# Kernel optimization log

Hardware: AMD Instinct MI355X
Metric: run time of the kernel (lower is better)

Reference implementation:

```python
import jax, jax.numpy as jnp
import numpy as np

S, B, H, E, V, L = 64, 32, 1024, 512, 32000, 2


def setup_inputs() -> dict:
    key = jax.random.key(0)
    ks = jax.random.split(key, 12)
    dl = 1.0 / float(np.sqrt(H))
    u = lambda k, shape, a: jax.random.uniform(k, shape, minval=-a, maxval=a, dtype=jnp.float32)
    return {
        "inputs": jax.random.randint(ks[0], (S, B), 0, V),            # token ids [seq, batch]
        "hidden": jnp.zeros((L, B, H), jnp.float32),                  # init_hidden()
        "emb_W": u(ks[1], (V, E), 0.1),                               # embedding, uniform(-0.1,0.1)
        "Wx0": u(ks[2], (H, E), dl), "Wh0": u(ks[3], (H, H), dl), "bh0": u(ks[4], (H,), dl),
        "Wx1": u(ks[5], (H, H), dl), "Wh1": u(ks[6], (H, H), dl), "bh1": u(ks[7], (H,), dl),
        "Wout": u(ks[8], (V, H), 0.1),                                # output Linear, uniform(-0.1,0.1)
        "bout": jnp.zeros((V,), jnp.float32),                         # output bias zeros
    }


def reference(inputs, hidden, emb_W, Wx0, Wh0, bh0, Wx1, Wh1, bh1, Wout, bout):
    # Embedding lookup for all timesteps (dropout is identity at dp_keep_prob=1.0)
    x = emb_W[inputs]  # [S, B, E]
    Wxs = (Wx0, Wx1)
    Whs = (Wh0, Wh1)
    bs = (bh0, bh1)

    def step(h, x_t):
        # h: [L, B, H]; x_t: [B, E]
        out = x_t
        new_h = []
        for j in range(L):  # fixed small number of structurally distinct layers
            hj = jnp.tanh(out @ Wxs[j].T + h[j] @ Whs[j].T + bs[j])  # vanilla tanh RNN cell
            new_h.append(hj)
            out = hj
        return jnp.stack(new_h), out

    hidden_final, tops = jax.lax.scan(step, hidden, x)  # tops: [S, B, H]
    logits = tops @ Wout.T + bout                        # [S, B, V]
    return logits, hidden_final
```

## Files before the change

### kernel.cpp

```cpp
#include <hip/hip_runtime.h>
#include <hip/hip_bf16.h>

#define S_ 64
#define B_ 32
#define H_ 1024
#define E_ 512
#define V_ 32000

typedef unsigned short ushort_t;
typedef __attribute__((ext_vector_type(8))) short short8;
typedef __attribute__((ext_vector_type(4))) float f32x4;

__device__ __forceinline__ ushort_t f32_bf16(float x) {
    union { float f; unsigned u; } v; v.f = x;
    unsigned r = v.u + 0x7FFF + ((v.u >> 16) & 1);
    return (ushort_t)(r >> 16);
}

__device__ __forceinline__ float bf16_f32(ushort_t x) {
    union { unsigned u; float f; } v; v.u = ((unsigned)x) << 16;
    return v.f;
}

__global__ void cvt_bf16(const float* __restrict__ src, ushort_t* __restrict__ dst, int n4) {
    int i = blockIdx.x * blockDim.x + threadIdx.x;
    int stride = gridDim.x * blockDim.x;
    const float4* s4 = (const float4*)src;
    ushort4* d4 = (ushort4*)dst;
    for (; i < n4; i += stride) {
        float4 v = s4[i];
        ushort4 o;
        o.x = f32_bf16(v.x); o.y = f32_bf16(v.y);
        o.z = f32_bf16(v.z); o.w = f32_bf16(v.w);
        d4[i] = o;
    }
}

__global__ void init_hidden(const float* __restrict__ hid,
                            ushort_t* __restrict__ h0buf, ushort_t* __restrict__ h1buf) {
    int i = blockIdx.x * blockDim.x + threadIdx.x;
    int j = i & (B_ * H_ - 1);
    if (i < B_ * H_) h0buf[B_ * H_ + j] = f32_bf16(hid[i]);
    else             h1buf[B_ * H_ + j] = f32_bf16(hid[i]);
}

__global__ void gather_emb(const int* __restrict__ tok, const float* __restrict__ emb,
                           ushort_t* __restrict__ xb) {
    int m = blockIdx.x;
    int t = tok[m];
    const float4* src = (const float4*)(emb + (long)t * E_);
    ushort4* dst = (ushort4*)(xb + (long)m * E_);
    int i = threadIdx.x;
    float4 v = src[i];
    ushort4 o;
    o.x = f32_bf16(v.x); o.y = f32_bf16(v.y);
    o.z = f32_bf16(v.z); o.w = f32_bf16(v.w);
    dst[i] = o;
}

__global__ __launch_bounds__(256) void xproj_kernel(const ushort_t* __restrict__ Xb,
                                                    const ushort_t* __restrict__ Wx0b,
                                                    const float* __restrict__ bh0,
                                                    float* __restrict__ xproj) {
    int wid = (blockIdx.x * 256 + threadIdx.x) >> 6;
    int lane = threadIdx.x & 63;
    int quad = lane >> 4;
    int nt = wid & 63, mt = wid >> 6;
    int mrow = mt * 16 + (lane & 15);
    int nrow = nt * 16 + (lane & 15);
    const short8* Ap = (const short8*)(Xb + (long)mrow * E_ + quad * 8);
    const short8* Bp = (const short8*)(Wx0b + (long)nrow * E_ + quad * 8);
    f32x4 acc = {0.f, 0.f, 0.f, 0.f};
#pragma unroll
    for (int k = 0; k < E_ / 32; ++k)
        acc = __builtin_amdgcn_mfma_f32_16x16x32_bf16(Ap[k * 4], Bp[k * 4], acc, 0, 0, 0);
    float bias = bh0[nrow];
#pragma unroll
    for (int r = 0; r < 4; ++r) {
        int m = mt * 16 + quad * 4 + r;
        xproj[(long)m * H_ + nrow] = acc[r] + bias;
    }
}

__global__ __launch_bounds__(256) void step_kernel(const ushort_t* __restrict__ Wh0b,
                                                   const ushort_t* __restrict__ Wx1b,
                                                   const ushort_t* __restrict__ Wh1b,
                                                   const float* __restrict__ bh1,
                                                   const float* __restrict__ xproj,
                                                   ushort_t* __restrict__ h0buf,
                                                   ushort_t* __restrict__ h1buf,
                                                   ushort_t* __restrict__ tops,
                                                   int p) {
    int lb = blockIdx.x;
    int lane = threadIdx.x & 63;
    int widx = threadIdx.x >> 6;
    int quad = lane >> 4;
    if (lb < 32) {
        if (p >= S_) return;
        int wid = lb * 4 + widx;
        int nt = wid & 63, mt = wid >> 6;
        int b0 = mt * 16 + (lane & 15);
        int h = nt * 16 + (lane & 15);
        const ushort_t* Aprev = h0buf + ((p + 1) & 1) * (B_ * H_);
        const short8* Ap = (const short8*)(Aprev + (long)b0 * H_ + quad * 8);
        const short8* Wp = (const short8*)(Wh0b + (long)h * H_ + quad * 8);
        f32x4 acc = {0.f, 0.f, 0.f, 0.f};
#pragma unroll
        for (int k = 0; k < H_ / 32; ++k)
            acc = __builtin_amdgcn_mfma_f32_16x16x32_bf16(Ap[k * 4], Wp[k * 4], acc, 0, 0, 0);
        ushort_t* out = h0buf + (p & 1) * (B_ * H_);
        const float* xp = xproj + (long)p * B_ * H_;
#pragma unroll
        for (int r = 0; r < 4; ++r) {
            int b = mt * 16 + quad * 4 + r;
            float v = tanhf(acc[r] + xp[b * H_ + h]);
            out[b * H_ + h] = f32_bf16(v);
        }
    } else {
        if (p < 1) return;
        int t = p - 1;
        int wid = (lb - 32) * 4 + widx;
        int nt = wid & 63, mt = wid >> 6;
        int b0 = mt * 16 + (lane & 15);
        int h = nt * 16 + (lane & 15);
        const ushort_t* A0 = h0buf + (t & 1) * (B_ * H_);
        const ushort_t* A1 = h1buf + ((t + 1) & 1) * (B_ * H_);
        const short8* Ap0 = (const short8*)(A0 + (long)b0 * H_ + quad * 8);
        const short8* Wp0 = (const short8*)(Wx1b + (long)h * H_ + quad * 8);
        const short8* Ap1 = (const short8*)(A1 + (long)b0 * H_ + quad * 8);
        const short8* Wp1 = (const short8*)(Wh1b + (long)h * H_ + quad * 8);
        f32x4 acc = {0.f, 0.f, 0.f, 0.f};
#pragma unroll
        for (int k = 0; k < H_ / 32; ++k)
            acc = __builtin_amdgcn_mfma_f32_16x16x32_bf16(Ap0[k * 4], Wp0[k * 4], acc, 0, 0, 0);
#pragma unroll
        for (int k = 0; k < H_ / 32; ++k)
            acc = __builtin_amdgcn_mfma_f32_16x16x32_bf16(Ap1[k * 4], Wp1[k * 4], acc, 0, 0, 0);
        float bias = bh1[h];
        ushort_t* out = h1buf + (t & 1) * (B_ * H_);
        ushort_t* top = tops + (long)t * B_ * H_;
#pragma unroll
        for (int r = 0; r < 4; ++r) {
            int b = mt * 16 + quad * 4 + r;
            float v = tanhf(acc[r] + bias);
            ushort_t bv = f32_bf16(v);
            out[b * H_ + h] = bv;
            top[b * H_ + h] = bv;
        }
    }
}

#define BM 128
#define BN 128
#define BK 32

__device__ __forceinline__ void ld_lds16(const ushort_t* g, ushort_t* l) {
    __builtin_amdgcn_global_load_lds((const __attribute__((address_space(1))) void*)g,
                                     (__attribute__((address_space(3))) void*)l, 16, 0, 0);
}

__global__ __launch_bounds__(256) void out_gemm(const ushort_t* __restrict__ A,
                                                const ushort_t* __restrict__ Bw,
                                                const float* __restrict__ bout,
                                                float* __restrict__ C) {
    __shared__ __align__(16) ushort_t lA[BM * BK];
    __shared__ __align__(16) ushort_t lB[BN * BK];
    int mblk = blockIdx.x;
    int nblk = blockIdx.y;
    int tid = threadIdx.x;
    int lane = tid & 63;
    int w = tid >> 6;
    int quad = lane >> 4;
    int srow = tid >> 2;
    int skol = (tid & 3) * 8;
    const ushort_t* Ag = A + (long)(mblk * BM + srow) * H_ + skol;
    const ushort_t* Bg = Bw + (long)(nblk * BN + srow) * H_ + skol;
    ushort_t* lA0 = lA + tid * 8;
    ushort_t* lA1 = lA + 2048 + tid * 8;
    ushort_t* lB0 = lB + tid * 8;
    ushort_t* lB1 = lB + 2048 + tid * 8;

    int msub = (w & 1) * 64;
    int nsub = (w >> 1) * 64;
    f32x4 acc[4][4];
#pragma unroll
    for (int i = 0; i < 4; ++i)
#pragma unroll
        for (int j = 0; j < 4; ++j) acc[i][j] = (f32x4){0.f, 0.f, 0.f, 0.f};

    for (int k0 = 0; k0 < H_; k0 += BK) {
        ld_lds16(Ag + k0, lA0);
        ld_lds16(Ag + 64 * H_ + k0, lA1);
        ld_lds16(Bg + k0, lB0);
        ld_lds16(Bg + 64 * H_ + k0, lB1);
        __syncthreads();
        short8 af[4], bf[4];
#pragma unroll
        for (int i = 0; i < 4; ++i)
            af[i] = *(const short8*)&lA[(msub + i * 16 + (lane & 15)) * BK + quad * 8];
#pragma unroll
        for (int j = 0; j < 4; ++j)
            bf[j] = *(const short8*)&lB[(nsub + j * 16 + (lane & 15)) * BK + quad * 8];
#pragma unroll
        for (int i = 0; i < 4; ++i)
#pragma unroll
            for (int j = 0; j < 4; ++j)
                acc[i][j] = __builtin_amdgcn_mfma_f32_16x16x32_bf16(af[i], bf[j], acc[i][j], 0, 0, 0);
        __syncthreads();
    }

#pragma unroll
    for (int j = 0; j < 4; ++j) {
        int n = nblk * BN + nsub + j * 16 + (lane & 15);
        float bo = bout[n];
#pragma unroll
        for (int i = 0; i < 4; ++i) {
#pragma unroll
            for (int r = 0; r < 4; ++r) {
                int m = mblk * BM + msub + i * 16 + quad * 4 + r;
                C[(long)m * V_ + n] = acc[i][j][r] + bo;
            }
        }
    }
}

__global__ void final_hidden(const ushort_t* __restrict__ h0buf,
                             const ushort_t* __restrict__ h1buf,
                             float* __restrict__ out) {
    int i = blockIdx.x * blockDim.x + threadIdx.x;
    int j = i & (B_ * H_ - 1);
    ushort_t v = (i < B_ * H_) ? h0buf[B_ * H_ + j] : h1buf[B_ * H_ + j];
    out[(long)S_ * B_ * V_ + i] = bf16_f32(v);
}

extern "C" void kernel_launch(void* const* d_in, const int* in_sizes, int n_in,
                              void* d_out, int out_size, void* d_ws, size_t ws_size,
                              hipStream_t stream) {
    const int*   tok  = (const int*)d_in[0];
    const float* hid  = (const float*)d_in[1];
    const float* emb  = (const float*)d_in[2];
    const float* Wx0  = (const float*)d_in[3];
    const float* Wh0  = (const float*)d_in[4];
    const float* bh0  = (const float*)d_in[5];
    const float* Wx1  = (const float*)d_in[6];
    const float* Wh1  = (const float*)d_in[7];
    const float* bh1  = (const float*)d_in[8];
    const float* Wout = (const float*)d_in[9];
    const float* bout = (const float*)d_in[10];
    float* out = (float*)d_out;

    char* ws = (char*)d_ws;
    size_t off = 0;
    ushort_t* woutb = (ushort_t*)(ws + off); off += (size_t)V_ * H_ * 2;
    ushort_t* wh0b  = (ushort_t*)(ws + off); off += (size_t)H_ * H_ * 2;
    ushort_t* wx1b  = (ushort_t*)(ws + off); off += (size_t)H_ * H_ * 2;
    ushort_t* wh1b  = (ushort_t*)(ws + off); off += (size_t)H_ * H_ * 2;
    ushort_t* wx0b  = (ushort_t*)(ws + off); off += (size_t)H_ * E_ * 2;
    ushort_t* xb    = (ushort_t*)(ws + off); off += (size_t)S_ * B_ * E_ * 2;
    float*    xproj = (float*)(ws + off);    off += (size_t)S_ * B_ * H_ * 4;
    ushort_t* topsb = (ushort_t*)(ws + off); off += (size_t)S_ * B_ * H_ * 2;
    ushort_t* h0b   = (ushort_t*)(ws + off); off += (size_t)2 * B_ * H_ * 2;
    ushort_t* h1b   = (ushort_t*)(ws + off); off += (size_t)2 * B_ * H_ * 2;

    cvt_bf16<<<2048, 256, 0, stream>>>(Wout, woutb, V_ * H_ / 4);
    cvt_bf16<<<256, 256, 0, stream>>>(Wh0, wh0b, H_ * H_ / 4);
    cvt_bf16<<<256, 256, 0, stream>>>(Wx1, wx1b, H_ * H_ / 4);
    cvt_bf16<<<256, 256, 0, stream>>>(Wh1, wh1b, H_ * H_ / 4);
    cvt_bf16<<<128, 256, 0, stream>>>(Wx0, wx0b, H_ * E_ / 4);
    init_hidden<<<256, 256, 0, stream>>>(hid, h0b, h1b);
    gather_emb<<<S_ * B_, 128, 0, stream>>>(tok, emb, xb);
    xproj_kernel<<<2048, 256, 0, stream>>>(xb, wx0b, bh0, xproj);
    for (int p = 0; p <= S_; ++p)
        step_kernel<<<64, 256, 0, stream>>>(wh0b, wx1b, wh1b, bh1, xproj, h0b, h1b, topsb, p);
    out_gemm<<<dim3(16, 250), 256, 0, stream>>>(topsb, woutb, bout, out);
    final_hidden<<<256, 256, 0, stream>>>(h0b, h1b, out);
}
```

Baseline: 1.674 ms.

## Fuse recurrent steps into one cooperative kernel and remap output GEMM blocks

Replaces the 65 per-timestep step_kernel launches with a single cooperative kernel that loops over timesteps and uses grid.sync between them, removing per-launch overhead. Weight pointers and bias are hoisted out of the loop. The output GEMM grid is flattened to 1D and blocks are remapped so consecutive workgroups are spread across groups of eight, likely to improve cache locality across XCDs. Grid-wide sync carries its own cost, and the kernel needs all 64 blocks resident at once.

Measured after the change: 2.042 ms. +22.0%, slower.

```diff
diff --git a/kernel.cpp b/kernel.cpp
--- a/kernel.cpp
+++ b/kernel.cpp
@@ -1,5 +1,8 @@
 #include <hip/hip_runtime.h>
 #include <hip/hip_bf16.h>
+#include <hip/hip_cooperative_groups.h>
+
+namespace cg = cooperative_groups;
 
 #define S_ 64
 #define B_ 32
@@ -82,71 +85,75 @@
     }
 }
 
-__global__ __launch_bounds__(256) void step_kernel(const ushort_t* __restrict__ Wh0b,
-                                                   const ushort_t* __restrict__ Wx1b,
-                                                   const ushort_t* __restrict__ Wh1b,
-                                                   const float* __restrict__ bh1,
-                                                   const float* __restrict__ xproj,
-                                                   ushort_t* __restrict__ h0buf,
-                                                   ushort_t* __restrict__ h1buf,
-                                                   ushort_t* __restrict__ tops,
-                                                   int p) {
-    int lb = blockIdx.x;
-    int lane = threadIdx.x & 63;
-    int widx = threadIdx.x >> 6;
-    int quad = lane >> 4;
-    if (lb < 32) {
-        if (p >= S_) return;
-        int wid = lb * 4 + widx;
-        int nt = wid & 63, mt = wid >> 6;
-        int b0 = mt * 16 + (lane & 15);
-        int h = nt * 16 + (lane & 15);
-        const ushort_t* Aprev = h0buf + ((p + 1) & 1) * (B_ * H_);
-        const short8* Ap = (const short8*)(Aprev + (long)b0 * H_ + quad * 8);
-        const short8* Wp = (const short8*)(Wh0b + (long)h * H_ + quad * 8);
-        f32x4 acc = {0.f, 0.f, 0.f, 0.f};
-#pragma unroll
-        for (int k = 0; k < H_ / 32; ++k)
-            acc = __builtin_amdgcn_mfma_f32_16x16x32_bf16(Ap[k * 4], Wp[k * 4], acc, 0, 0, 0);
-        ushort_t* out = h0buf + (p & 1) * (B_ * H_);
-        const float* xp = xproj + (long)p * B_ * H_;
-#pragma unroll
-        for (int r = 0; r < 4; ++r) {
-            int b = mt * 16 + quad * 4 + r;
-            float v = tanhf(acc[r] + xp[b * H_ + h]);
-            out[b * H_ + h] = f32_bf16(v);
+__global__ __launch_bounds__(256) void rnn_steps(const ushort_t* __restrict__ Wh0b,
+                                                 const ushort_t* __restrict__ Wx1b,
+                                                 const ushort_t* __restrict__ Wh1b,
+                                                 const float* __restrict__ bh1,
+                                                 const float* __restrict__ xproj,
+                                                 ushort_t* __restrict__ h0buf,
+                                                 ushort_t* __restrict__ h1buf,
+                                                 ushort_t* __restrict__ tops) {
+    cg::grid_group grid = cg::this_grid();
+    const int lb = blockIdx.x;
+    const int lane = threadIdx.x & 63;
+    const int widx = threadIdx.x >> 6;
+    const int quad = lane >> 4;
+    const int wid = (lb & 31) * 4 + widx;
+    const int nt = wid & 63, mt = wid >> 6;
+    const int b0 = mt * 16 + (lane & 15);
+    const int h = nt * 16 + (lane & 15);
+    const bool is_l0 = (lb < 32);
+
+    const short8* Wp  = (const short8*)(Wh0b + (long)h * H_ + quad * 8);
+    const short8* Wp0 = (const short8*)(Wx1b + (long)h * H_ + quad * 8);
+    const short8* Wp1 = (const short8*)(Wh1b + (long)h * H_ + quad * 8);
+    const float bias1 = bh1[h];
+
+    for (int p = 0; p <= S_; ++p) {
+        if (is_l0) {
+            if (p < S_) {
+                const ushort_t* Aprev = h0buf + ((p + 1) & 1) * (B_ * H_);
+                const short8* Ap = (const short8*)(Aprev + (long)b0 * H_ + quad * 8);
+                f32x4 acc = {0.f, 0.f, 0.f, 0.f};
+#pragma unroll
+                for (int k = 0; k < H_ / 32; ++k)
+                    acc = __builtin_amdgcn_mfma_f32_16x16x32_bf16(Ap[k * 4], Wp[k * 4], acc, 0, 0, 0);
+                ushort_t* out = h0buf + (p & 1) * (B_ * H_);
+                const float* xp = xproj + (long)p * B_ * H_;
+#pragma unroll
+                for (int r = 0; r < 4; ++r) {
+                    int b = mt * 16 + quad * 4 + r;
+                    float v = tanhf(acc[r] + xp[b * H_ + h]);
+                    out[b * H_ + h] = f32_bf16(v);
+                }
+            }
+        } else {
+            if (p >= 1) {
+                int t = p - 1;
+                const ushort_t* A0 = h0buf + (t & 1) * (B_ * H_);
+                const ushort_t* A1 = h1buf + ((t + 1) & 1) * (B_ * H_);
+                const short8* Ap0 = (const short8*)(A0 + (long)b0 * H_ + quad * 8);
+                const short8* Ap1 = (const short8*)(A1 + (long)b0 * H_ + quad * 8);
+                f32x4 acc = {0.f, 0.f, 0.f, 0.f};
+#pragma unroll
+                for (int k = 0; k < H_ / 32; ++k)
+                    acc = __builtin_amdgcn_mfma_f32_16x16x32_bf16(Ap0[k * 4], Wp0[k * 4], acc, 0, 0, 0);
+#pragma unroll
+                for (int k = 0; k < H_ / 32; ++k)
+                    acc = __builtin_amdgcn_mfma_f32_16x16x32_bf16(Ap1[k * 4], Wp1[k * 4], acc, 0, 0, 0);
+                ushort_t* out = h1buf + (t & 1) * (B_ * H_);
+                ushort_t* top = tops + (long)t * B_ * H_;
+#pragma unroll
+                for (int r = 0; r < 4; ++r) {
+                    int b = mt * 16 + quad * 4 + r;
+                    float v = tanhf(acc[r] + bias1);
+                    ushort_t bv = f32_bf16(v);
+                    out[b * H_ + h] = bv;
+                    top[b * H_ + h] = bv;
+                }
+            }
         }
-    } else {
-        if (p < 1) return;
-        int t = p - 1;
-        int wid = (lb - 32) * 4 + widx;
-        int nt = wid & 63, mt = wid >> 6;
-        int b0 = mt * 16 + (lane & 15);
-        int h = nt * 16 + (lane & 15);
-        const ushort_t* A0 = h0buf + (t & 1) * (B_ * H_);
-        const ushort_t* A1 = h1buf + ((t + 1) & 1) * (B_ * H_);
-        const short8* Ap0 = (const short8*)(A0 + (long)b0 * H_ + quad * 8);
-        const short8* Wp0 = (const short8*)(Wx1b + (long)h * H_ + quad * 8);
-        const short8* Ap1 = (const short8*)(A1 + (long)b0 * H_ + quad * 8);
-        const short8* Wp1 = (const short8*)(Wh1b + (long)h * H_ + quad * 8);
-        f32x4 acc = {0.f, 0.f, 0.f, 0.f};
-#pragma unroll
-        for (int k = 0; k < H_ / 32; ++k)
-            acc = __builtin_amdgcn_mfma_f32_16x16x32_bf16(Ap0[k * 4], Wp0[k * 4], acc, 0, 0, 0);
-#pragma unroll
-        for (int k = 0; k < H_ / 32; ++k)
-            acc = __builtin_amdgcn_mfma_f32_16x16x32_bf16(Ap1[k * 4], Wp1[k * 4], acc, 0, 0, 0);
-        float bias = bh1[h];
-        ushort_t* out = h1buf + (t & 1) * (B_ * H_);
-        ushort_t* top = tops + (long)t * B_ * H_;
-#pragma unroll
-        for (int r = 0; r < 4; ++r) {
-            int b = mt * 16 + quad * 4 + r;
-            float v = tanhf(acc[r] + bias);
-            ushort_t bv = f32_bf16(v);
-            out[b * H_ + h] = bv;
-            top[b * H_ + h] = bv;
-        }
+        if (p < S_) grid.sync();
     }
 }
 
@@ -165,8 +172,10 @@
                                                 float* __restrict__ C) {
     __shared__ __align__(16) ushort_t lA[BM * BK];
     __shared__ __align__(16) ushort_t lB[BN * BK];
-    int mblk = blockIdx.x;
-    int nblk = blockIdx.y;
+    int orig = blockIdx.x;
+    int wgid = (orig & 7) * 500 + (orig >> 3);
+    int mblk = wgid & 15;
+    int nblk = wgid >> 4;
     int tid = threadIdx.x;
     int lane = tid & 63;
     int w = tid >> 6;
@@ -270,8 +279,11 @@
     init_hidden<<<256, 256, 0, stream>>>(hid, h0b, h1b);
     gather_emb<<<S_ * B_, 128, 0, stream>>>(tok, emb, xb);
     xproj_kernel<<<2048, 256, 0, stream>>>(xb, wx0b, bh0, xproj);
-    for (int p = 0; p <= S_; ++p)
-        step_kernel<<<64, 256, 0, stream>>>(wh0b, wx1b, wh1b, bh1, xproj, h0b, h1b, topsb, p);
-    out_gemm<<<dim3(16, 250), 256, 0, stream>>>(topsb, woutb, bout, out);
+    {
+        void* args[] = {(void*)&wh0b, (void*)&wx1b, (void*)&wh1b, (void*)&bh1,
+                        (void*)&xproj, (void*)&h0b, (void*)&h1b, (void*)&topsb};
+        hipLaunchCooperativeKernel((const void*)rnn_steps, dim3(64), dim3(256), args, 0u, stream);
+    }
+    out_gemm<<<4000, 256, 0, stream>>>(topsb, woutb, bout, out);
     final_hidden<<<256, 256, 0, stream>>>(h0b, h1b, out);
 }
```
